# Kernel optimization log

Hardware: AMD Instinct MI355X
Metric: run time of the kernel (lower is better)

The kernel has to match this reference:

```python
import jax, jax.numpy as jnp
import numpy as np

L_SEQ = 4096   # sequence length L
E = 1024       # embedding_size
NL = 8         # num_layers
H = 4 * E      # channel-mix hidden
V = 4          # LocalHilDim
LOGP_FACTOR = 0.5


def setup_inputs() -> dict:
    key = jax.random.key(0)
    ks = jax.random.split(key, 20)
    n = lambda k, shp, s=0.02: jax.random.normal(k, shp, jnp.float32) * s
    u = lambda k, shp: jax.random.uniform(k, shp, dtype=jnp.float32)
    return {
        "s": jax.random.randint(ks[0], (L_SEQ,), 0, V),
        "embed": n(ks[1], (V, E), 1.0),
        # TimeMixing params, stacked over layers
        "tm_first": jnp.log(jnp.float32(0.3)) + n(ks[2], (NL, E), 0.5),
        "tm_decay": -5.0 + 8.0 * u(ks[3], (NL, E)),
        "tm_mk": u(ks[4], (NL, E)),
        "tm_mv": u(ks[5], (NL, E)),
        "tm_mr": u(ks[6], (NL, E)),
        "tm_Wk": n(ks[7], (NL, E, E)),
        "tm_Wv": n(ks[8], (NL, E, E)),
        "tm_Wr": n(ks[9], (NL, E, E)),
        "tm_Wo": n(ks[10], (NL, E, E)),
        # ChannelMixing params
        "cm_mk": u(ks[11], (NL, E)),
        "cm_mr": u(ks[12], (NL, E)),
        "cm_Wk": n(ks[13], (NL, E, H)),
        "cm_Wr": n(ks[14], (NL, E, E)),
        "cm_Wv": n(ks[15], (NL, H, E)),
        # Neck / Head
        "neck_W": n(ks[16], (E, E)),
        "neck_b": jnp.zeros((E,), jnp.float32),
        "head_W": n(ks[17], (E, V)),
    }


def _wkv(k, v, time_first, time_decay):
    """Max-stabilized RWKV WKV recurrence over time. k,v: [L,E]."""
    z = jnp.zeros_like(k[0])
    init = (z, z, jnp.full_like(k[0], -jnp.inf))  # aa, bb, pp

    def step(carry, kv):
        aa, bb, pp = carry
        kk, vv = kv
        ww = time_first + kk
        p = jnp.maximum(pp, ww)
        e1 = jnp.exp(pp - p)
        e2 = jnp.exp(ww - p)
        out = (e1 * aa + e2 * vv) / (e1 * bb + e2)
        ww = pp - jnp.exp(time_decay)
        p = jnp.maximum(ww, kk)
        e1 = jnp.exp(ww - p)
        e2 = jnp.exp(kk - p)
        return (e1 * aa + e2 * vv, e1 * bb + e2, p), out

    _, out = jax.lax.scan(step, init, (k, v))
    return out


def _shift(x):
    # prepend zero-state row, drop last (token-shift with zero initial state)
    return jnp.concatenate([jnp.zeros_like(x[:1]), x[:-1]], axis=0)


def _block(x, p):
    # --- TimeMixing ---
    sx = _shift(x)
    kx = x * p["tm_mk"] + sx * (1 - p["tm_mk"])
    vx = x * p["tm_mv"] + sx * (1 - p["tm_mv"])
    rx = x * p["tm_mr"] + sx * (1 - p["tm_mr"])
    r = jax.nn.sigmoid(rx @ p["tm_Wr"])
    k = kx @ p["tm_Wk"]
    v = vx @ p["tm_Wv"]
    wkv = _wkv(k, v, p["tm_first"], p["tm_decay"])
    x = x + (r * wkv) @ p["tm_Wo"]
    # --- ChannelMixing ---
    sx = _shift(x)
    xk = x * p["cm_mk"] + sx * (1 - p["cm_mk"])
    xr = x * p["cm_mr"] + sx * (1 - p["cm_mr"])
    r = jax.nn.sigmoid(xr @ p["cm_Wr"])
    kk = jnp.square(jax.nn.relu(xk @ p["cm_Wk"]))  # [L, 4E]
    x = x + r * (kk @ p["cm_Wv"])
    return x


def reference(s, embed, tm_first, tm_decay, tm_mk, tm_mv, tm_mr,
              tm_Wk, tm_Wv, tm_Wr, tm_Wo, cm_mk, cm_mr, cm_Wk, cm_Wr, cm_Wv,
              neck_W, neck_b, head_W):
    tok = jnp.pad(s[:-1], (1, 0))
    x = embed[tok]                          # [L, E]
    layer_params = {
        "tm_first": tm_first, "tm_decay": tm_decay,
        "tm_mk": tm_mk, "tm_mv": tm_mv, "tm_mr": tm_mr,
        "tm_Wk": tm_Wk, "tm_Wv": tm_Wv, "tm_Wr": tm_Wr, "tm_Wo": tm_Wo,
        "cm_mk": cm_mk, "cm_mr": cm_mr,
        "cm_Wk": cm_Wk, "cm_Wr": cm_Wr, "cm_Wv": cm_Wv,
    }

    def body(x, p):
        return _block(x, p), None

    x, _ = jax.lax.scan(body, x, layer_params)  # scan over NL layers
    x = jax.nn.gelu(x @ neck_W + neck_b)
    logits = x @ head_W                         # [L, V]
    logp = jax.nn.log_softmax(logits) * LOGP_FACTOR
    # log-amplitude of configuration s (Q is None -> no mask, no penalty)
    return jnp.take_along_axis(logp, s[:, None], axis=-1).sum(axis=-2).squeeze(-1)
```

## Files before the change

kernel.cpp:

```cpp
#include <hip/hip_runtime.h>
#include <stdint.h>

#define L_SEQ 4096
#define EDIM  1024
#define HDIM  4096
#define NLAY  8
#define WKV_C 128
#define WKV_T 32
#define SCAN_LANES 16
#define SCAN_CPT   (WKV_C / SCAN_LANES)

typedef unsigned short u16;
typedef __attribute__((ext_vector_type(8))) short short8;
typedef __attribute__((ext_vector_type(4))) float f32x4;
typedef __attribute__((ext_vector_type(4))) unsigned short us4;

static __device__ __forceinline__ u16 f2b(float f) {
  union { float f; uint32_t u; } a; a.f = f;
  uint32_t u = a.u;
  return (u16)((u + 0x7FFFu + ((u >> 16) & 1u)) >> 16);
}
static __device__ __forceinline__ float b2f(u16 b) {
  union { uint32_t u; float f; } a; a.u = ((uint32_t)b) << 16;
  return a.f;
}
static __device__ __forceinline__ float sigm(float v) {
  return 1.f / (1.f + __expf(-v));
}
static __device__ __forceinline__ float4 ld_bf4(const u16* __restrict__ p, size_t i) {
  us4 v = *reinterpret_cast<const us4*>(&p[i]);
  return make_float4(b2f(v.x), b2f(v.y), b2f(v.z), b2f(v.w));
}

static __device__ __forceinline__ void gld_lds16(const void* g, void* l) {
  __builtin_amdgcn_global_load_lds(
      (const __attribute__((address_space(1))) void*)g,
      (__attribute__((address_space(3))) void*)l, 16, 0, 0);
}


__global__ void k_f0(const int* __restrict__ s, const float* __restrict__ embed,
                     const float* __restrict__ mk, const float* __restrict__ mv,
                     const float* __restrict__ mr, float* __restrict__ xA,
                     u16* __restrict__ kx, u16* __restrict__ vx, u16* __restrict__ rx) {
  int i = (blockIdx.x * blockDim.x + threadIdx.x) * 4;
  int t = i >> 10, e = i & 1023;
  int tok = (t == 0) ? 0 : s[t - 1];
  float4 xc = *reinterpret_cast<const float4*>(&embed[tok * EDIM + e]);
  float4 xs = make_float4(0.f, 0.f, 0.f, 0.f);
  if (t > 0) {
    int tokp = (t == 1) ? 0 : s[t - 2];
    xs = *reinterpret_cast<const float4*>(&embed[tokp * EDIM + e]);
  }
  *reinterpret_cast<float4*>(&xA[i]) = xc;
  float4 m; us4 o;
  m = *reinterpret_cast<const float4*>(&mk[e]);
  o.x = f2b(xc.x * m.x + xs.x * (1.f - m.x)); o.y = f2b(xc.y * m.y + xs.y * (1.f - m.y));
  o.z = f2b(xc.z * m.z + xs.z * (1.f - m.z)); o.w = f2b(xc.w * m.w + xs.w * (1.f - m.w));
  *reinterpret_cast<us4*>(&kx[i]) = o;
  m = *reinterpret_cast<const float4*>(&mv[e]);
  o.x = f2b(xc.x * m.x + xs.x * (1.f - m.x)); o.y = f2b(xc.y * m.y + xs.y * (1.f - m.y));
  o.z = f2b(xc.z * m.z + xs.z * (1.f - m.z)); o.w = f2b(xc.w * m.w + xs.w * (1.f - m.w));
  *reinterpret_cast<us4*>(&vx[i]) = o;
  m = *reinterpret_cast<const float4*>(&mr[e]);
  o.x = f2b(xc.x * m.x + xs.x * (1.f - m.x)); o.y = f2b(xc.y * m.y + xs.y * (1.f - m.y));
  o.z = f2b(xc.z * m.z + xs.z * (1.f - m.z)); o.w = f2b(xc.w * m.w + xs.w * (1.f - m.w));
  *reinterpret_cast<us4*>(&rx[i]) = o;
}

static __device__ __forceinline__ float4 cm_finish(const float* __restrict__ xB,
                                                   const u16* __restrict__ PR,
                                                   const u16* __restrict__ PB, int i) {
  const size_t LE = (size_t)L_SEQ * EDIM;
  float4 xm = *reinterpret_cast<const float4*>(&xB[i]);
  float4 r0 = ld_bf4(PR, i), r1 = ld_bf4(PR, i + LE);
  float4 v0 = ld_bf4(PB, i), v1 = ld_bf4(PB, i + LE);
  float4 v2 = ld_bf4(PB, i + 2 * LE), v3 = ld_bf4(PB, i + 3 * LE);
  xm.x += sigm(r0.x + r1.x) * (v0.x + v1.x + v2.x + v3.x);
  xm.y += sigm(r0.y + r1.y) * (v0.y + v1.y + v2.y + v3.y);
  xm.z += sigm(r0.z + r1.z) * (v0.z + v1.z + v2.z + v3.z);
  xm.w += sigm(r0.w + r1.w) * (v0.w + v1.w + v2.w + v3.w);
  return xm;
}

__global__ void k_f1(const float* __restrict__ xB, const u16* __restrict__ PR,
                     const u16* __restrict__ PB,
                     const float* __restrict__ mk, const float* __restrict__ mv,
                     const float* __restrict__ mr, float* __restrict__ xA,
                     u16* __restrict__ kx, u16* __restrict__ vx, u16* __restrict__ rx) {
  int i = (blockIdx.x * blockDim.x + threadIdx.x) * 4;
  int e = i & 1023;
  float4 xc = cm_finish(xB, PR, PB, i);
  float4 xs = make_float4(0.f, 0.f, 0.f, 0.f);
  if (i >= EDIM) xs = cm_finish(xB, PR, PB, i - EDIM);
  *reinterpret_cast<float4*>(&xA[i]) = xc;
  float4 m; us4 o;
  m = *reinterpret_cast<const float4*>(&mk[e]);
  o.x = f2b(xc.x * m.x + xs.x * (1.f - m.x)); o.y = f2b(xc.y * m.y + xs.y * (1.f - m.y));
  o.z = f2b(xc.z * m.z + xs.z * (1.f - m.z)); o.w = f2b(xc.w * m.w + xs.w * (1.f - m.w));
  *reinterpret_cast<us4*>(&kx[i]) = o;
  m = *reinterpret_cast<const float4*>(&mv[e]);
  o.x = f2b(xc.x * m.x + xs.x * (1.f - m.x)); o.y = f2b(xc.y * m.y + xs.y * (1.f - m.y));
  o.z = f2b(xc.z * m.z + xs.z * (1.f - m.z)); o.w = f2b(xc.w * m.w + xs.w * (1.f - m.w));
  *reinterpret_cast<us4*>(&vx[i]) = o;
  m = *reinterpret_cast<const float4*>(&mr[e]);
  o.x = f2b(xc.x * m.x + xs.x * (1.f - m.x)); o.y = f2b(xc.y * m.y + xs.y * (1.f - m.y));
  o.z = f2b(xc.z * m.z + xs.z * (1.f - m.z)); o.w = f2b(xc.w * m.w + xs.w * (1.f - m.w));
  *reinterpret_cast<us4*>(&rx[i]) = o;
}

static __device__ __forceinline__ float4 tm_finish(const float* __restrict__ xA,
                                                   const u16* __restrict__ PA, int i) {
  const size_t LE = (size_t)L_SEQ * EDIM;
  float4 xm = *reinterpret_cast<const float4*>(&xA[i]);
  float4 a = ld_bf4(PA, i), b = ld_bf4(PA, i + LE);
  xm.x += a.x + b.x; xm.y += a.y + b.y; xm.z += a.z + b.z; xm.w += a.w + b.w;
  return xm;
}

__global__ void k_f2(const float* __restrict__ xA, const u16* __restrict__ PA,
                     const float* __restrict__ mk, const float* __restrict__ mr,
                     float* __restrict__ xB, u16* __restrict__ kx, u16* __restrict__ rx) {
  int i = (blockIdx.x * blockDim.x + threadIdx.x) * 4;
  int e = i & 1023;
  float4 xc = tm_finish(xA, PA, i);
  float4 xs = make_float4(0.f, 0.f, 0.f, 0.f);
  if (i >= EDIM) xs = tm_finish(xA, PA, i - EDIM);
  *reinterpret_cast<float4*>(&xB[i]) = xc;
  float4 m; us4 o;
  m = *reinterpret_cast<const float4*>(&mk[e]);
  o.x = f2b(xc.x * m.x + xs.x * (1.f - m.x)); o.y = f2b(xc.y * m.y + xs.y * (1.f - m.y));
  o.z = f2b(xc.z * m.z + xs.z * (1.f - m.z)); o.w = f2b(xc.w * m.w + xs.w * (1.f - m.w));
  *reinterpret_cast<us4*>(&kx[i]) = o;
  m = *reinterpret_cast<const float4*>(&mr[e]);
  o.x = f2b(xc.x * m.x + xs.x * (1.f - m.x)); o.y = f2b(xc.y * m.y + xs.y * (1.f - m.y));
  o.z = f2b(xc.z * m.z + xs.z * (1.f - m.z)); o.w = f2b(xc.w * m.w + xs.w * (1.f - m.w));
  *reinterpret_cast<us4*>(&rx[i]) = o;
}

__global__ void k_f3(const float* __restrict__ xB, const u16* __restrict__ PR,
                     const u16* __restrict__ PB, u16* __restrict__ hb) {
  int i = (blockIdx.x * blockDim.x + threadIdx.x) * 4;
  float4 xc = cm_finish(xB, PR, PB, i);
  us4 o;
  o.x = f2b(xc.x); o.y = f2b(xc.y); o.z = f2b(xc.z); o.w = f2b(xc.w);
  *reinterpret_cast<us4*>(&hb[i]) = o;
}

static __device__ __forceinline__ float gelu1(float v) {
  float c = 0.7978845608028654f * (v + 0.044715f * v * v * v);
  return 0.5f * v * (1.f + tanhf(c));
}

static __device__ __forceinline__
void tconv_body(const float* __restrict__ s, u16* __restrict__ d, int K, int N) {
  __shared__ float tile[64][65];
  int n0 = blockIdx.x * 64, k0 = blockIdx.y * 64;
  int tx = threadIdx.x & 15, ty = threadIdx.x >> 4;
#pragma unroll
  for (int i = 0; i < 4; ++i) {
    int kr = ty + i * 16;
    float4 v = *reinterpret_cast<const float4*>(&s[(size_t)(k0 + kr) * N + n0 + tx * 4]);
    tile[kr][tx * 4 + 0] = v.x; tile[kr][tx * 4 + 1] = v.y;
    tile[kr][tx * 4 + 2] = v.z; tile[kr][tx * 4 + 3] = v.w;
  }
  __syncthreads();
#pragma unroll
  for (int i = 0; i < 4; ++i) {
    int nr = ty + i * 16;
    us4 o;
    o.x = f2b(tile[tx * 4 + 0][nr]); o.y = f2b(tile[tx * 4 + 1][nr]);
    o.z = f2b(tile[tx * 4 + 2][nr]); o.w = f2b(tile[tx * 4 + 3][nr]);
    *reinterpret_cast<us4*>(&d[(size_t)(n0 + nr) * K + k0 + tx * 4]) = o;
  }
}

__global__ __launch_bounds__(256)
void k_tconv(const float* __restrict__ src, u16* __restrict__ dst, int K, int N) {
  tconv_body(src + (size_t)blockIdx.z * K * N, dst + (size_t)blockIdx.z * K * N, K, N);
}

__global__ __launch_bounds__(256)
void k_tconv_ee(const float* __restrict__ Wk, const float* __restrict__ Wv,
                const float* __restrict__ Wr, const float* __restrict__ Wo,
                const float* __restrict__ cWr, const float* __restrict__ nW,
                u16* __restrict__ oWk, u16* __restrict__ oWv, u16* __restrict__ oWr,
                u16* __restrict__ oWo, u16* __restrict__ ocWr, u16* __restrict__ onW) {
  const size_t EE = (size_t)EDIM * EDIM;
  int z = blockIdx.z;
  const float* src; u16* dst;
  if (z < 8)       { src = Wk  + (size_t)z * EE;        dst = oWk  + (size_t)z * EE; }
  else if (z < 16) { src = Wv  + (size_t)(z - 8) * EE;  dst = oWv  + (size_t)(z - 8) * EE; }
  else if (z < 24) { src = Wr  + (size_t)(z - 16) * EE; dst = oWr  + (size_t)(z - 16) * EE; }
  else if (z < 32) { src = Wo  + (size_t)(z - 24) * EE; dst = oWo  + (size_t)(z - 24) * EE; }
  else if (z < 40) { src = cWr + (size_t)(z - 32) * EE; dst = ocWr + (size_t)(z - 32) * EE; }
  else             { src = nW;                          dst = onW; }
  tconv_body(src, dst, EDIM, EDIM);
}

template <int EPI>
__device__ __forceinline__
void g256_body(const u16* __restrict__ A, const u16* __restrict__ Bt,
               void* __restrict__ Cv, int N, int ldk, int klen,
               int bm, int bn) {
  extern __shared__ __align__(16) u16 lds[];
  const int tid = threadIdx.x, lane = tid & 63, w = tid >> 6;
  const int wr = w >> 2, wc = w & 3;
  const int l16 = lane & 15, lhi = lane >> 4;
  const int NT = klen >> 5;

  f32x4 acc[8][4];
#pragma unroll
  for (int i = 0; i < 8; ++i)
#pragma unroll
    for (int j = 0; j < 4; ++j)
#pragma unroll
      for (int r = 0; r < 4; ++r) acc[i][j][r] = 0.f;

  const int sd = tid * 16;
  const int sr = sd >> 6;
  const int sc = ((sd >> 4) & 3) ^ ((sr >> 1) & 3);
  const int sdst = w * 512;

  const int spn = lhi ^ ((l16 >> 1) & 3);
  const int aBase = wr * 4096 + l16 * 32 + spn * 8;
  const int bBase = 8192 + (wc >> 1) * 4096 + ((wc & 1) * 64 + l16) * 32 + spn * 8;

  auto stage_ht = [&](int kt, int ht) {
    const u16* src = (ht < 2) ? A : Bt;
    int rowbase = ((ht < 2) ? bm : bn) + (ht & 1) * 128;
    gld_lds16(src + (size_t)(rowbase + sr) * ldk + kt * 32 + sc * 8,
              &lds[(kt & 3) * 16384 + ht * 4096 + sdst]);
  };

#pragma unroll
  for (int t = 0; t < 3; ++t)
#pragma unroll
    for (int h = 0; h < 4; ++h) stage_ht(t, h);
  asm volatile("s_waitcnt vmcnt(8)" ::: "memory");
  __builtin_amdgcn_s_barrier();

  short8 a[4], b[4];
  for (int kt = 0; kt < NT; ++kt) {
    const int pb = (kt & 3) * 16384;
    __builtin_amdgcn_sched_barrier(0);
#pragma unroll
    for (int mi = 0; mi < 4; ++mi)
      a[mi] = *reinterpret_cast<const short8*>(&lds[pb + aBase + mi * 512]);
#pragma unroll
    for (int ni = 0; ni < 4; ++ni)
      b[ni] = *reinterpret_cast<const short8*>(&lds[pb + bBase + ni * 512]);
    if (kt + 3 < NT) { stage_ht(kt + 3, 0); stage_ht(kt + 3, 1); }
    __builtin_amdgcn_s_barrier();
    asm volatile("s_waitcnt lgkmcnt(0)" ::: "memory");
    __builtin_amdgcn_sched_barrier(0);
    __builtin_amdgcn_s_setprio(1);
#pragma unroll
    for (int mi = 0; mi < 4; ++mi)
#pragma unroll
      for (int ni = 0; ni < 4; ++ni)
        acc[mi][ni] = __builtin_amdgcn_mfma_f32_16x16x32_bf16(a[mi], b[ni], acc[mi][ni], 0, 0, 0);
    __builtin_amdgcn_s_setprio(0);
    __builtin_amdgcn_s_barrier();
    __builtin_amdgcn_sched_barrier(0);
#pragma unroll
    for (int mi = 0; mi < 4; ++mi)
      a[mi] = *reinterpret_cast<const short8*>(&lds[pb + aBase + 2048 + mi * 512]);
    if (kt + 3 < NT) { stage_ht(kt + 3, 2); stage_ht(kt + 3, 3); }
    __builtin_amdgcn_s_barrier();
    asm volatile("s_waitcnt lgkmcnt(0)" ::: "memory");
    __builtin_amdgcn_sched_barrier(0);
    __builtin_amdgcn_s_setprio(1);
#pragma unroll
    for (int mi = 0; mi < 4; ++mi)
#pragma unroll
      for (int ni = 0; ni < 4; ++ni)
        acc[4 + mi][ni] = __builtin_amdgcn_mfma_f32_16x16x32_bf16(a[mi], b[ni], acc[4 + mi][ni], 0, 0, 0);
    __builtin_amdgcn_s_setprio(0);
    if (kt + 4 <= NT)      asm volatile("s_waitcnt vmcnt(8)" ::: "memory");
    else if (kt + 3 == NT) asm volatile("s_waitcnt vmcnt(4)" ::: "memory");
    else if (kt + 2 == NT) asm volatile("s_waitcnt vmcnt(0)" ::: "memory");
    __builtin_amdgcn_s_barrier();
  }

#pragma unroll
  for (int q = 0; q < 8; ++q)
#pragma unroll
    for (int ni = 0; ni < 4; ++ni)
#pragma unroll
      for (int r = 0; r < 4; ++r) {
        int row = bm + wr * 128 + (q >> 2) * 64 + (q & 3) * 16 + lhi * 4 + r;
        int col = bn + wc * 64 + ni * 16 + l16;
        size_t o = (size_t)row * N + col;
        float v = acc[q][ni][r];
        if constexpr (EPI == 0) ((float*)Cv)[o] = v;
        else if constexpr (EPI == 1) ((u16*)Cv)[o] = f2b(v);
        else { v = fmaxf(v, 0.f); ((u16*)Cv)[o] = f2b(v * v); }
      }
}

__global__ __launch_bounds__(512)
void k_g256_cmk(const u16* __restrict__ A, const u16* __restrict__ Bt,
                u16* __restrict__ C) {
  int bid = blockIdx.x;
  int wg = (bid & 7) * 32 + (bid >> 3);
  int lb = wg & 3, sv = wg >> 2;
  int by = (sv >> 3) * 2 + (lb & 1);
  int bx = (sv & 7) * 2 + (lb >> 1);
  g256_body<2>(A, Bt, C, HDIM, EDIM, EDIM, by * 256, bx * 256);
}

__global__ __launch_bounds__(512)
void k_g256_wv(const u16* __restrict__ A, const u16* __restrict__ Bt,
               u16* __restrict__ P) {
  int bid = blockIdx.x;
  int wg = (bid & 7) * 32 + (bid >> 3);
  int z = wg >> 6, rem = wg & 63;
  int lb = rem & 3, sv = rem >> 2;
  int by = (sv >> 1) * 2 + (lb & 1);
  int bx = (sv & 1) * 2 + (lb >> 1);
  g256_body<1>(A + z * 1024, Bt + z * 1024, P + (size_t)z * L_SEQ * EDIM,
               EDIM, HDIM, 1024, by * 256, bx * 256);
}

__global__ __launch_bounds__(512)
void k_g256_3(const u16* __restrict__ A0, const u16* __restrict__ A1, const u16* __restrict__ A2,
              const u16* __restrict__ B0, const u16* __restrict__ B1, const u16* __restrict__ B2,
              u16* __restrict__ C0, u16* __restrict__ C1, u16* __restrict__ C2) {
  int bid = blockIdx.x;
  int wg = (bid & 7) * 24 + (bid >> 3);
  int z = wg >> 6, rem = wg & 63;
  int lb = rem & 3, sv = rem >> 2;
  int by = (sv >> 1) * 2 + (lb & 1);
  int bx = (sv & 1) * 2 + (lb >> 1);
  const u16* A = (z == 0) ? A0 : (z == 1) ? A1 : A2;
  const u16* B = (z == 0) ? B0 : (z == 1) ? B1 : B2;
  u16*       C = (z == 0) ? C0 : (z == 1) ? C1 : C2;
  g256_body<1>(A, B, C, EDIM, EDIM, EDIM, by * 256, bx * 256);
}

__device__ __forceinline__
void gemm_body(const u16* __restrict__ A, const u16* __restrict__ Bt,
               u16* __restrict__ Cv, int N, int ldk, int klen, int bm, int bn) {
  __shared__ __align__(16) u16 As[4][128 * 32];
  __shared__ __align__(16) u16 Bs[4][128 * 32];
  const int tid = threadIdx.x, lane = tid & 63, w = tid >> 6;
  const int wr = w >> 1, wc = w & 1;
  const int l16 = lane & 15, lhi = lane >> 4;

  f32x4 acc[4][4];
#pragma unroll
  for (int a = 0; a < 4; ++a)
#pragma unroll
    for (int b = 0; b < 4; ++b)
#pragma unroll
      for (int r = 0; r < 4; ++r) acc[a][b][r] = 0.f;

  const size_t rowBytes = (size_t)ldk * 2;
  const int NT = klen >> 5;

  int srow[2], scb[2], ldso[2];
#pragma unroll
  for (int i = 0; i < 2; ++i) {
    int off = w * 2048 + i * 1024 + lane * 16;
    int r = off >> 6, sl = (off >> 4) & 3;
    srow[i] = r;
    scb[i] = ((sl - (r >> 1)) & 3) << 4;
    ldso[i] = (w * 2048 + i * 1024) >> 1;
  }

  auto stage = [&](int t, int buf) {
    int kb = t * 64;
#pragma unroll
    for (int i = 0; i < 2; ++i) {
      gld_lds16((const char*)A + (size_t)(bm + srow[i]) * rowBytes + kb + scb[i],
                &As[buf][ldso[i]]);
      gld_lds16((const char*)Bt + (size_t)(bn + srow[i]) * rowBytes + kb + scb[i],
                &Bs[buf][ldso[i]]);
    }
  };

  int aoff[4], boff[4];
#pragma unroll
  for (int mi = 0; mi < 4; ++mi) {
    int r = wr * 64 + mi * 16 + l16;
    aoff[mi] = r * 32 + (((lhi + (r >> 1)) & 3) << 3);
    r = wc * 64 + mi * 16 + l16;
    boff[mi] = r * 32 + (((lhi + (r >> 1)) & 3) << 3);
  }

  stage(0, 0); stage(1, 1); stage(2, 2);
  for (int t = 0; t < NT; ++t) {
    const int cur = t & 3;
    if (t + 2 < NT)      asm volatile("s_waitcnt vmcnt(8)" ::: "memory");
    else if (t + 1 < NT) asm volatile("s_waitcnt vmcnt(4)" ::: "memory");
    else                 asm volatile("s_waitcnt vmcnt(0)" ::: "memory");
    __builtin_amdgcn_s_barrier();
    __builtin_amdgcn_sched_barrier(0);
    short8 af[4], bfr[4];
#pragma unroll
    for (int mi = 0; mi < 4; ++mi)
      af[mi] = *reinterpret_cast<const short8*>(&As[cur][aoff[mi]]);
#pragma unroll
    for (int ni = 0; ni < 4; ++ni)
      bfr[ni] = *reinterpret_cast<const short8*>(&Bs[cur][boff[ni]]);
    if (t + 3 < NT) stage(t + 3, (t + 3) & 3);
    asm volatile("s_waitcnt lgkmcnt(0)" ::: "memory");
    __builtin_amdgcn_sched_barrier(0);
#pragma unroll
    for (int mi = 0; mi < 4; ++mi)
#pragma unroll
      for (int ni = 0; ni < 4; ++ni)
        acc[mi][ni] = __builtin_amdgcn_mfma_f32_16x16x32_bf16(af[mi], bfr[ni], acc[mi][ni], 0, 0, 0);
  }
#pragma unroll
  for (int mi = 0; mi < 4; ++mi)
#pragma unroll
    for (int ni = 0; ni < 4; ++ni)
#pragma unroll
      for (int r = 0; r < 4; ++r) {
        int row = bm + wr * 64 + mi * 16 + lhi * 4 + r;
        int col = bn + wc * 64 + ni * 16 + l16;
        Cv[(size_t)row * N + col] = f2b(acc[mi][ni][r]);
      }
}

__global__ __launch_bounds__(256)
void k_gemm_sk2(const u16* __restrict__ A, const u16* __restrict__ Bt,
                u16* __restrict__ P, int K) {
  const int z = blockIdx.z, klen = K >> 1;
  gemm_body(A + z * klen, Bt + z * klen, P + (size_t)z * L_SEQ * EDIM,
            EDIM, K, klen, blockIdx.y * 128, blockIdx.x * 128);
}


__global__ void k_wkv_pass1(const u16* __restrict__ k, const u16* __restrict__ v,
                            const float* __restrict__ w_,
                            float* __restrict__ sa, float* __restrict__ sb,
                            float* __restrict__ sp) {
  int id = blockIdx.x * blockDim.x + threadIdx.x;
  int e = id & 1023, c = id >> 10;
  float D = __expf(w_[e]);
  float aa = 0.f, bb = 0.f, pp = -__builtin_inff();
  const u16* kp = k + (size_t)c * WKV_T * EDIM + e;
  const u16* vp = v + (size_t)c * WKV_T * EDIM + e;
#pragma unroll 4
  for (int i = 0; i < WKV_T; ++i) {
    float kk = b2f(kp[i * EDIM]), vv = b2f(vp[i * EDIM]);
    float ww = pp - D;
    float p2 = fmaxf(ww, kk);
    float e1 = __expf(ww - p2), e2 = __expf(kk - p2);
    aa = e1 * aa + e2 * vv;
    bb = e1 * bb + e2;
    pp = p2;
  }
  sa[id] = aa; sb[id] = bb; sp[id] = pp;
}

__global__ __launch_bounds__(256)
void k_wkv_scan16(const float* __restrict__ w_,
                  const float* __restrict__ sa, const float* __restrict__ sb,
                  const float* __restrict__ sp,
                  float* __restrict__ oa, float* __restrict__ ob,
                  float* __restrict__ op) {
  int t = blockIdx.x * blockDim.x + threadIdx.x;
  int e = t >> 4, j = t & (SCAN_LANES - 1);
  const float NEG = -1e30f;
  float DT = __expf(w_[e]) * (float)WKV_T;
  float Ea[SCAN_CPT], Eb[SCAN_CPT], Ep[SCAN_CPT];
  float A = 0.f, B = 0.f, P = NEG;
  int base = j * SCAN_CPT;
#pragma unroll
  for (int i = 0; i < SCAN_CPT; ++i) {
    int idx = (base + i) * EDIM + e;
    Ea[i] = A; Eb[i] = B; Ep[i] = P;
    float a = sa[idx], b = sb[idx], q = sp[idx];
    float shift = P - DT;
    float pn = fmaxf(shift, q);
    float w1 = __expf(shift - pn), w2 = __expf(q - pn);
    A = w1 * A + w2 * a; B = w1 * B + w2 * b; P = pn;
  }
  float tA = A, tB = B, tP = P; int tn = SCAN_CPT;
#pragma unroll
  for (int d = 1; d < SCAN_LANES; d <<= 1) {
    float fA = __shfl_up(tA, d, SCAN_LANES);
    float fB = __shfl_up(tB, d, SCAN_LANES);
    float fP = __shfl_up(tP, d, SCAN_LANES);
    int   fn = __shfl_up(tn, d, SCAN_LANES);
    if (j >= d) {
      float shift = fP - DT * (float)tn;
      float pn = fmaxf(shift, tP);
      float w1 = __expf(shift - pn), w2 = __expf(tP - pn);
      tA = w1 * fA + w2 * tA; tB = w1 * fB + w2 * tB; tP = pn; tn += fn;
    }
  }
  float pA = __shfl_up(tA, 1, SCAN_LANES);
  float pB = __shfl_up(tB, 1, SCAN_LANES);
  float pP = __shfl_up(tP, 1, SCAN_LANES);
  if (j == 0) { pA = 0.f; pB = 0.f; pP = NEG; }
#pragma unroll
  for (int i = 0; i < SCAN_CPT; ++i) {
    float shift = pP - DT * (float)i;
    float pn = fmaxf(shift, Ep[i]);
    float w1 = __expf(shift - pn), w2 = __expf(Ep[i] - pn);
    int idx = (base + i) * EDIM + e;
    oa[idx] = w1 * pA + w2 * Ea[i];
    ob[idx] = w1 * pB + w2 * Eb[i];
    op[idx] = pn;
  }
}

__global__ void k_wkv_pass2(const u16* __restrict__ k, const u16* __restrict__ v,
                            const float* __restrict__ u_, const float* __restrict__ w_,
                            const float* __restrict__ sa, const float* __restrict__ sb,
                            const float* __restrict__ sp,
                            const u16* __restrict__ rpre, u16* __restrict__ rwb) {
  int id = blockIdx.x * blockDim.x + threadIdx.x;
  int e = id & 1023, c = id >> 10;
  float u = u_[e];
  float D = __expf(w_[e]);
  float aa = sa[id], bb = sb[id], pp = sp[id];
  const size_t base = (size_t)c * WKV_T * EDIM + e;
  const u16* kp = k + base;
  const u16* vp = v + base;
  const u16* rp = rpre + base;
  u16* op = rwb + base;
#pragma unroll 4
  for (int i = 0; i < WKV_T; ++i) {
    float kk = b2f(kp[i * EDIM]), vv = b2f(vp[i * EDIM]);
    float ww = u + kk;
    float p = fmaxf(pp, ww);
    float e1 = __expf(pp - p), e2 = __expf(ww - p);
    float out = (e1 * aa + e2 * vv) / (e1 * bb + e2);
    op[i * EDIM] = f2b(out * sigm(b2f(rp[i * EDIM])));
    float w2s = pp - D;
    float p2 = fmaxf(w2s, kk);
    float e1b = __expf(w2s - p2), e2b = __expf(kk - p2);
    aa = e1b * aa + e2b * vv;
    bb = e1b * bb + e2b;
    pp = p2;
  }
}

__global__ __launch_bounds__(256)
void k_head(const u16* __restrict__ P, const float* __restrict__ nb,
            const float* __restrict__ W,
            const int* __restrict__ s, float* __restrict__ partial) {
  const size_t LE = (size_t)L_SEQ * EDIM;
  int t = blockIdx.x, tid = threadIdx.x;
  float a0 = 0.f, a1 = 0.f, a2 = 0.f, a3 = 0.f;
  for (int e = tid; e < EDIM; e += 256) {
    size_t i = (size_t)t * EDIM + e;
    float hv = gelu1(b2f(P[i]) + b2f(P[i + LE]) + nb[e]);
    const float4 wv = *reinterpret_cast<const float4*>(W + e * 4);
    a0 += hv * wv.x; a1 += hv * wv.y; a2 += hv * wv.z; a3 += hv * wv.w;
  }
#pragma unroll
  for (int off = 32; off > 0; off >>= 1) {
    a0 += __shfl_down(a0, off, 64);
    a1 += __shfl_down(a1, off, 64);
    a2 += __shfl_down(a2, off, 64);
    a3 += __shfl_down(a3, off, 64);
  }
  __shared__ float sm[4][4];
  int w = tid >> 6, lane = tid & 63;
  if (lane == 0) { sm[w][0] = a0; sm[w][1] = a1; sm[w][2] = a2; sm[w][3] = a3; }
  __syncthreads();
  if (tid == 0) {
    float lg[4];
#pragma unroll
    for (int j = 0; j < 4; ++j) lg[j] = sm[0][j] + sm[1][j] + sm[2][j] + sm[3][j];
    float m = fmaxf(fmaxf(lg[0], lg[1]), fmaxf(lg[2], lg[3]));
    float sum = expf(lg[0] - m) + expf(lg[1] - m) + expf(lg[2] - m) + expf(lg[3] - m);
    partial[t] = 0.5f * (lg[s[t]] - m - logf(sum));
  }
}

__global__ __launch_bounds__(256)
void k_reduce(const float* __restrict__ partial, float* __restrict__ out) {
  int tid = threadIdx.x;
  float a = 0.f;
  for (int j = tid; j < L_SEQ; j += 256) a += partial[j];
#pragma unroll
  for (int off = 32; off > 0; off >>= 1) a += __shfl_down(a, off, 64);
  __shared__ float sm[4];
  if ((tid & 63) == 0) sm[tid >> 6] = a;
  __syncthreads();
  if (tid == 0) out[0] = sm[0] + sm[1] + sm[2] + sm[3];
}


extern "C" void kernel_launch(void* const* d_in, const int* in_sizes, int n_in,
                              void* d_out, int out_size, void* d_ws, size_t ws_size,
                              hipStream_t stream) {
  const int*   s        = (const int*)d_in[0];
  const float* embed    = (const float*)d_in[1];
  const float* tm_first = (const float*)d_in[2];
  const float* tm_decay = (const float*)d_in[3];
  const float* tm_mk    = (const float*)d_in[4];
  const float* tm_mv    = (const float*)d_in[5];
  const float* tm_mr    = (const float*)d_in[6];
  const float* tm_Wk    = (const float*)d_in[7];
  const float* tm_Wv    = (const float*)d_in[8];
  const float* tm_Wr    = (const float*)d_in[9];
  const float* tm_Wo    = (const float*)d_in[10];
  const float* cm_mk    = (const float*)d_in[11];
  const float* cm_mr    = (const float*)d_in[12];
  const float* cm_Wk    = (const float*)d_in[13];
  const float* cm_Wr    = (const float*)d_in[14];
  const float* cm_Wv    = (const float*)d_in[15];
  const float* neck_W   = (const float*)d_in[16];
  const float* neck_b   = (const float*)d_in[17];
  const float* head_W   = (const float*)d_in[18];

  char* ws = (char*)d_ws;
  size_t off = 0;
  auto alloc = [&](size_t bytes) { char* p = ws + off; off += (bytes + 255) & ~(size_t)255; return p; };
  const size_t LE4 = (size_t)L_SEQ * EDIM * 4, LE2 = (size_t)L_SEQ * EDIM * 2;
  const size_t EE  = (size_t)EDIM * EDIM, EH = (size_t)EDIM * HDIM;

  float* xA    = (float*)alloc(LE4);
  float* xB    = (float*)alloc(LE4);
  u16*   kxb   = (u16*)alloc(LE2);
  u16*   vxb   = (u16*)alloc(LE2);
  u16*   rxb   = (u16*)alloc(LE2);
  u16*   kf    = (u16*)alloc(LE2);
  u16*   vf    = (u16*)alloc(LE2);
  u16*   rpre  = (u16*)alloc(LE2);
  u16*   kkb   = (u16*)alloc((size_t)L_SEQ * HDIM * 2);
  u16*   PA    = (u16*)alloc(2 * LE2);
  u16*   PR    = (u16*)alloc(2 * LE2);
  u16*   PB    = (u16*)alloc(4 * LE2);
  float* partial = (float*)alloc((size_t)L_SEQ * 4);
  float* sa  = (float*)alloc((size_t)WKV_C * EDIM * 4);
  float* sb  = (float*)alloc((size_t)WKV_C * EDIM * 4);
  float* sp  = (float*)alloc((size_t)WKV_C * EDIM * 4);
  float* sa2 = (float*)alloc((size_t)WKV_C * EDIM * 4);
  float* sb2 = (float*)alloc((size_t)WKV_C * EDIM * 4);
  float* sp2 = (float*)alloc((size_t)WKV_C * EDIM * 4);

  size_t remain = (ws_size > off) ? ws_size - off : 0;
  const size_t bigNeed = (5 * EE * NLAY + 2 * EH * NLAY + EE) * 2 + 16 * 256;
  const bool big = remain >= bigNeed;
  const int NB = big ? NLAY : 1;
  u16* wWk   = (u16*)alloc(EE * NB * 2);
  u16* wWv   = (u16*)alloc(EE * NB * 2);
  u16* wWr   = (u16*)alloc(EE * NB * 2);
  u16* wWo   = (u16*)alloc(EE * NB * 2);
  u16* wcmWr = (u16*)alloc(EE * NB * 2);
  u16* wcmWk = (u16*)alloc(EH * NB * 2);
  u16* wcmWv = (u16*)alloc(EH * NB * 2);
  u16* wneck = big ? (u16*)alloc(EE * 2) : wWk;

  const dim3 blk(256);
  const dim3 blk512(512);
  const dim3 gE4((L_SEQ * EDIM) / 1024);
  const dim3 gemmSK(EDIM / 128, L_SEQ / 128, 2);
  const dim3 gWkv((WKV_C * EDIM) / 256);
  const dim3 gScan((EDIM * SCAN_LANES) / 256);
  const size_t DLDS = 131072;

  if (big) {
    k_tconv_ee<<<dim3(EDIM / 64, EDIM / 64, 41), blk, 0, stream>>>(
        tm_Wk, tm_Wv, tm_Wr, tm_Wo, cm_Wr, neck_W,
        wWk, wWv, wWr, wWo, wcmWr, wneck);
    k_tconv<<<dim3(HDIM / 64, EDIM / 64, NLAY), blk, 0, stream>>>(cm_Wk, wcmWk, EDIM, HDIM);
    k_tconv<<<dim3(EDIM / 64, HDIM / 64, NLAY), blk, 0, stream>>>(cm_Wv, wcmWv, HDIM, EDIM);
  }

  for (int l = 0; l < NLAY; ++l) {
    size_t oE  = (size_t)l * EDIM;
    size_t oEE = (size_t)l * EE;
    size_t oEH = (size_t)l * EH;
    size_t wE  = big ? oEE : 0;
    size_t wH  = big ? oEH : 0;
    if (!big) {
      k_tconv<<<dim3(EDIM / 64, EDIM / 64, 1), blk, 0, stream>>>(tm_Wk + oEE, wWk, EDIM, EDIM);
      k_tconv<<<dim3(EDIM / 64, EDIM / 64, 1), blk, 0, stream>>>(tm_Wv + oEE, wWv, EDIM, EDIM);
      k_tconv<<<dim3(EDIM / 64, EDIM / 64, 1), blk, 0, stream>>>(tm_Wr + oEE, wWr, EDIM, EDIM);
      k_tconv<<<dim3(EDIM / 64, EDIM / 64, 1), blk, 0, stream>>>(tm_Wo + oEE, wWo, EDIM, EDIM);
      k_tconv<<<dim3(EDIM / 64, EDIM / 64, 1), blk, 0, stream>>>(cm_Wr + oEE, wcmWr, EDIM, EDIM);
      k_tconv<<<dim3(HDIM / 64, EDIM / 64, 1), blk, 0, stream>>>(cm_Wk + oEH, wcmWk, EDIM, HDIM);
      k_tconv<<<dim3(EDIM / 64, HDIM / 64, 1), blk, 0, stream>>>(cm_Wv + oEH, wcmWv, HDIM, EDIM);
    }
    if (l == 0)
      k_f0<<<gE4, blk, 0, stream>>>(s, embed, tm_mk + oE, tm_mv + oE, tm_mr + oE,
                                    xA, kxb, vxb, rxb);
    else
      k_f1<<<gE4, blk, 0, stream>>>(xB, PR, PB, tm_mk + oE, tm_mv + oE, tm_mr + oE,
                                    xA, kxb, vxb, rxb);
    k_g256_3<<<dim3(192), blk512, DLDS, stream>>>(kxb, vxb, rxb,
                                                  wWk + wE, wWv + wE, wWr + wE,
                                                  kf, vf, rpre);
    k_wkv_pass1<<<gWkv, blk, 0, stream>>>(kf, vf, tm_decay + oE, sa, sb, sp);
    k_wkv_scan16<<<gScan, blk, 0, stream>>>(tm_decay + oE, sa, sb, sp, sa2, sb2, sp2);
    k_wkv_pass2<<<gWkv, blk, 0, stream>>>(kf, vf, tm_first + oE, tm_decay + oE,
                                          sa2, sb2, sp2, rpre, vxb);
    k_gemm_sk2<<<gemmSK, blk, 0, stream>>>(vxb, wWo + wE, PA, EDIM);
    k_f2<<<gE4, blk, 0, stream>>>(xA, PA, cm_mk + oE, cm_mr + oE, xB, kxb, rxb);
    k_gemm_sk2<<<gemmSK, blk, 0, stream>>>(rxb, wcmWr + wE, PR, EDIM);
    k_g256_cmk<<<dim3(256), blk512, DLDS, stream>>>(kxb, wcmWk + wH, kkb);
    k_g256_wv<<<dim3(256), blk512, DLDS, stream>>>(kkb, wcmWv + wH, PB);
  }
  if (!big) k_tconv<<<dim3(EDIM / 64, EDIM / 64, 1), blk, 0, stream>>>(neck_W, wneck, EDIM, EDIM);
  k_f3<<<gE4, blk, 0, stream>>>(xB, PR, PB, kxb);
  k_gemm_sk2<<<gemmSK, blk, 0, stream>>>(kxb, wneck, PA, EDIM);
  k_head<<<dim3(L_SEQ), blk, 0, stream>>>(PA, neck_b, head_W, s, partial);
  k_reduce<<<dim3(1), blk, 0, stream>>>(partial, (float*)d_out);

  (void)in_sizes; (void)n_in; (void)out_size;
}
```

Measured before the change: 1.888 ms.

## Store residual stream in bf16 and merge weight transpose-convert launches

The fp32 residual buffers xA/xB become bf16, which halves their global traffic in the elementwise finish kernels. The three weight transpose/convert launches are merged into one flat-grid kernel, and its store path now writes 8-wide bf16 vectors instead of 4-wide. In exchange, the residual stream is rounded to bf16 after every sublayer across all 8 layers, which adds accumulated rounding error and may threaten the accuracy tolerance.

```diff
diff --git a/kernel.cpp b/kernel.cpp
--- a/kernel.cpp
+++ b/kernel.cpp
@@ -14,6 +14,7 @@
 typedef __attribute__((ext_vector_type(8))) short short8;
 typedef __attribute__((ext_vector_type(4))) float f32x4;
 typedef __attribute__((ext_vector_type(4))) unsigned short us4;
+typedef __attribute__((ext_vector_type(8))) unsigned short us8;
 
 static __device__ __forceinline__ u16 f2b(float f) {
   union { float f; uint32_t u; } a; a.f = f;
@@ -41,7 +42,7 @@
 
 __global__ void k_f0(const int* __restrict__ s, const float* __restrict__ embed,
                      const float* __restrict__ mk, const float* __restrict__ mv,
-                     const float* __restrict__ mr, float* __restrict__ xA,
+                     const float* __restrict__ mr, u16* __restrict__ xA,
                      u16* __restrict__ kx, u16* __restrict__ vx, u16* __restrict__ rx) {
   int i = (blockIdx.x * blockDim.x + threadIdx.x) * 4;
   int t = i >> 10, e = i & 1023;
@@ -52,7 +53,8 @@
     int tokp = (t == 1) ? 0 : s[t - 2];
     xs = *reinterpret_cast<const float4*>(&embed[tokp * EDIM + e]);
   }
-  *reinterpret_cast<float4*>(&xA[i]) = xc;
+  us4 ox; ox.x = f2b(xc.x); ox.y = f2b(xc.y); ox.z = f2b(xc.z); ox.w = f2b(xc.w);
+  *reinterpret_cast<us4*>(&xA[i]) = ox;
   float4 m; us4 o;
   m = *reinterpret_cast<const float4*>(&mk[e]);
   o.x = f2b(xc.x * m.x + xs.x * (1.f - m.x)); o.y = f2b(xc.y * m.y + xs.y * (1.f - m.y));
@@ -68,11 +70,11 @@
   *reinterpret_cast<us4*>(&rx[i]) = o;
 }
 
-static __device__ __forceinline__ float4 cm_finish(const float* __restrict__ xB,
+static __device__ __forceinline__ float4 cm_finish(const u16* __restrict__ xB,
                                                    const u16* __restrict__ PR,
                                                    const u16* __restrict__ PB, int i) {
   const size_t LE = (size_t)L_SEQ * EDIM;
-  float4 xm = *reinterpret_cast<const float4*>(&xB[i]);
+  float4 xm = ld_bf4(xB, i);
   float4 r0 = ld_bf4(PR, i), r1 = ld_bf4(PR, i + LE);
   float4 v0 = ld_bf4(PB, i), v1 = ld_bf4(PB, i + LE);
   float4 v2 = ld_bf4(PB, i + 2 * LE), v3 = ld_bf4(PB, i + 3 * LE);
@@ -83,17 +85,18 @@
   return xm;
 }
 
-__global__ void k_f1(const float* __restrict__ xB, const u16* __restrict__ PR,
+__global__ void k_f1(const u16* __restrict__ xB, const u16* __restrict__ PR,
                      const u16* __restrict__ PB,
                      const float* __restrict__ mk, const float* __restrict__ mv,
-                     const float* __restrict__ mr, float* __restrict__ xA,
+                     const float* __restrict__ mr, u16* __restrict__ xA,
                      u16* __restrict__ kx, u16* __restrict__ vx, u16* __restrict__ rx) {
   int i = (blockIdx.x * blockDim.x + threadIdx.x) * 4;
   int e = i & 1023;
   float4 xc = cm_finish(xB, PR, PB, i);
   float4 xs = make_float4(0.f, 0.f, 0.f, 0.f);
   if (i >= EDIM) xs = cm_finish(xB, PR, PB, i - EDIM);
-  *reinterpret_cast<float4*>(&xA[i]) = xc;
+  us4 ox; ox.x = f2b(xc.x); ox.y = f2b(xc.y); ox.z = f2b(xc.z); ox.w = f2b(xc.w);
+  *reinterpret_cast<us4*>(&xA[i]) = ox;
   float4 m; us4 o;
   m = *reinterpret_cast<const float4*>(&mk[e]);
   o.x = f2b(xc.x * m.x + xs.x * (1.f - m.x)); o.y = f2b(xc.y * m.y + xs.y * (1.f - m.y));
@@ -109,24 +112,25 @@
   *reinterpret_cast<us4*>(&rx[i]) = o;
 }
 
-static __device__ __forceinline__ float4 tm_finish(const float* __restrict__ xA,
+static __device__ __forceinline__ float4 tm_finish(const u16* __restrict__ xA,
                                                    const u16* __restrict__ PA, int i) {
   const size_t LE = (size_t)L_SEQ * EDIM;
-  float4 xm = *reinterpret_cast<const float4*>(&xA[i]);
+  float4 xm = ld_bf4(xA, i);
   float4 a = ld_bf4(PA, i), b = ld_bf4(PA, i + LE);
   xm.x += a.x + b.x; xm.y += a.y + b.y; xm.z += a.z + b.z; xm.w += a.w + b.w;
   return xm;
 }
 
-__global__ void k_f2(const float* __restrict__ xA, const u16* __restrict__ PA,
+__global__ void k_f2(const u16* __restrict__ xA, const u16* __restrict__ PA,
                      const float* __restrict__ mk, const float* __restrict__ mr,
-                     float* __restrict__ xB, u16* __restrict__ kx, u16* __restrict__ rx) {
+                     u16* __restrict__ xB, u16* __restrict__ kx, u16* __restrict__ rx) {
   int i = (blockIdx.x * blockDim.x + threadIdx.x) * 4;
   int e = i & 1023;
   float4 xc = tm_finish(xA, PA, i);
   float4 xs = make_float4(0.f, 0.f, 0.f, 0.f);
   if (i >= EDIM) xs = tm_finish(xA, PA, i - EDIM);
-  *reinterpret_cast<float4*>(&xB[i]) = xc;
+  us4 ox; ox.x = f2b(xc.x); ox.y = f2b(xc.y); ox.z = f2b(xc.z); ox.w = f2b(xc.w);
+  *reinterpret_cast<us4*>(&xB[i]) = ox;
   float4 m; us4 o;
   m = *reinterpret_cast<const float4*>(&mk[e]);
   o.x = f2b(xc.x * m.x + xs.x * (1.f - m.x)); o.y = f2b(xc.y * m.y + xs.y * (1.f - m.y));
@@ -138,7 +142,7 @@
   *reinterpret_cast<us4*>(&rx[i]) = o;
 }
 
-__global__ void k_f3(const float* __restrict__ xB, const u16* __restrict__ PR,
+__global__ void k_f3(const u16* __restrict__ xB, const u16* __restrict__ PR,
                      const u16* __restrict__ PB, u16* __restrict__ hb) {
   int i = (blockIdx.x * blockDim.x + threadIdx.x) * 4;
   float4 xc = cm_finish(xB, PR, PB, i);
@@ -153,10 +157,11 @@
 }
 
 static __device__ __forceinline__
-void tconv_body(const float* __restrict__ s, u16* __restrict__ d, int K, int N) {
+void tconv2(const float* __restrict__ s, u16* __restrict__ d, int K, int N,
+            int n0, int k0) {
   __shared__ float tile[64][65];
-  int n0 = blockIdx.x * 64, k0 = blockIdx.y * 64;
-  int tx = threadIdx.x & 15, ty = threadIdx.x >> 4;
+  int tid = threadIdx.x;
+  int tx = tid & 15, ty = tid >> 4;
 #pragma unroll
   for (int i = 0; i < 4; ++i) {
     int kr = ty + i * 16;
@@ -165,37 +170,56 @@
     tile[kr][tx * 4 + 2] = v.z; tile[kr][tx * 4 + 3] = v.w;
   }
   __syncthreads();
-#pragma unroll
-  for (int i = 0; i < 4; ++i) {
-    int nr = ty + i * 16;
-    us4 o;
-    o.x = f2b(tile[tx * 4 + 0][nr]); o.y = f2b(tile[tx * 4 + 1][nr]);
-    o.z = f2b(tile[tx * 4 + 2][nr]); o.w = f2b(tile[tx * 4 + 3][nr]);
-    *reinterpret_cast<us4*>(&d[(size_t)(n0 + nr) * K + k0 + tx * 4]) = o;
+  int tx8 = tid & 7, ny = tid >> 3;
+#pragma unroll
+  for (int h = 0; h < 2; ++h) {
+    int n = ny + h * 32;
+    us8 o;
+#pragma unroll
+    for (int c = 0; c < 8; ++c) o[c] = f2b(tile[tx8 * 8 + c][n]);
+    *reinterpret_cast<us8*>(&d[(size_t)(n0 + n) * K + k0 + tx8 * 8]) = o;
   }
 }
 
 __global__ __launch_bounds__(256)
 void k_tconv(const float* __restrict__ src, u16* __restrict__ dst, int K, int N) {
-  tconv_body(src + (size_t)blockIdx.z * K * N, dst + (size_t)blockIdx.z * K * N, K, N);
-}
-
+  tconv2(src + (size_t)blockIdx.z * K * N, dst + (size_t)blockIdx.z * K * N,
+         K, N, blockIdx.x * 64, blockIdx.y * 64);
+}
+
+#define TC_EE  (41 * 256)
+#define TC_EH  8192
 __global__ __launch_bounds__(256)
-void k_tconv_ee(const float* __restrict__ Wk, const float* __restrict__ Wv,
-                const float* __restrict__ Wr, const float* __restrict__ Wo,
-                const float* __restrict__ cWr, const float* __restrict__ nW,
-                u16* __restrict__ oWk, u16* __restrict__ oWv, u16* __restrict__ oWr,
-                u16* __restrict__ oWo, u16* __restrict__ ocWr, u16* __restrict__ onW) {
-  const size_t EE = (size_t)EDIM * EDIM;
-  int z = blockIdx.z;
-  const float* src; u16* dst;
-  if (z < 8)       { src = Wk  + (size_t)z * EE;        dst = oWk  + (size_t)z * EE; }
-  else if (z < 16) { src = Wv  + (size_t)(z - 8) * EE;  dst = oWv  + (size_t)(z - 8) * EE; }
-  else if (z < 24) { src = Wr  + (size_t)(z - 16) * EE; dst = oWr  + (size_t)(z - 16) * EE; }
-  else if (z < 32) { src = Wo  + (size_t)(z - 24) * EE; dst = oWo  + (size_t)(z - 24) * EE; }
-  else if (z < 40) { src = cWr + (size_t)(z - 32) * EE; dst = ocWr + (size_t)(z - 32) * EE; }
-  else             { src = nW;                          dst = onW; }
-  tconv_body(src, dst, EDIM, EDIM);
+void k_tconv_all(const float* __restrict__ Wk, const float* __restrict__ Wv,
+                 const float* __restrict__ Wr, const float* __restrict__ Wo,
+                 const float* __restrict__ cWr, const float* __restrict__ nW,
+                 const float* __restrict__ cWk, const float* __restrict__ cWv,
+                 u16* __restrict__ oWk, u16* __restrict__ oWv, u16* __restrict__ oWr,
+                 u16* __restrict__ oWo, u16* __restrict__ ocWr, u16* __restrict__ onW,
+                 u16* __restrict__ ocWk, u16* __restrict__ ocWv) {
+  const size_t EE = (size_t)EDIM * EDIM, EH = (size_t)EDIM * HDIM;
+  int bid = blockIdx.x;
+  if (bid < TC_EE) {
+    int z = bid >> 8, rem = bid & 255;
+    const float* src; u16* dst;
+    if (z < 8)       { src = Wk  + (size_t)z * EE;        dst = oWk  + (size_t)z * EE; }
+    else if (z < 16) { src = Wv  + (size_t)(z - 8) * EE;  dst = oWv  + (size_t)(z - 8) * EE; }
+    else if (z < 24) { src = Wr  + (size_t)(z - 16) * EE; dst = oWr  + (size_t)(z - 16) * EE; }
+    else if (z < 32) { src = Wo  + (size_t)(z - 24) * EE; dst = oWo  + (size_t)(z - 24) * EE; }
+    else if (z < 40) { src = cWr + (size_t)(z - 32) * EE; dst = ocWr + (size_t)(z - 32) * EE; }
+    else             { src = nW;                          dst = onW; }
+    tconv2(src, dst, EDIM, EDIM, (rem & 15) * 64, (rem >> 4) * 64);
+  } else if (bid < TC_EE + TC_EH) {
+    int b = bid - TC_EE;
+    int z = b >> 10, rem = b & 1023;
+    tconv2(cWk + (size_t)z * EH, ocWk + (size_t)z * EH, EDIM, HDIM,
+           (rem & 63) * 64, (rem >> 6) * 64);
+  } else {
+    int b = bid - TC_EE - TC_EH;
+    int z = b >> 10, rem = b & 1023;
+    tconv2(cWv + (size_t)z * EH, ocWv + (size_t)z * EH, HDIM, EDIM,
+           (rem & 15) * 64, (rem >> 4) * 64);
+  }
 }
 
 template <int EPI>
@@ -616,11 +640,11 @@
   char* ws = (char*)d_ws;
   size_t off = 0;
   auto alloc = [&](size_t bytes) { char* p = ws + off; off += (bytes + 255) & ~(size_t)255; return p; };
-  const size_t LE4 = (size_t)L_SEQ * EDIM * 4, LE2 = (size_t)L_SEQ * EDIM * 2;
+  const size_t LE2 = (size_t)L_SEQ * EDIM * 2;
   const size_t EE  = (size_t)EDIM * EDIM, EH = (size_t)EDIM * HDIM;
 
-  float* xA    = (float*)alloc(LE4);
-  float* xB    = (float*)alloc(LE4);
+  u16*   xA    = (u16*)alloc(LE2);
+  u16*   xB    = (u16*)alloc(LE2);
   u16*   kxb   = (u16*)alloc(LE2);
   u16*   vxb   = (u16*)alloc(LE2);
   u16*   rxb   = (u16*)alloc(LE2);
@@ -661,11 +685,9 @@
   const size_t DLDS = 131072;
 
   if (big) {
-    k_tconv_ee<<<dim3(EDIM / 64, EDIM / 64, 41), blk, 0, stream>>>(
-        tm_Wk, tm_Wv, tm_Wr, tm_Wo, cm_Wr, neck_W,
-        wWk, wWv, wWr, wWo, wcmWr, wneck);
-    k_tconv<<<dim3(HDIM / 64, EDIM / 64, NLAY), blk, 0, stream>>>(cm_Wk, wcmWk, EDIM, HDIM);
-    k_tconv<<<dim3(EDIM / 64, HDIM / 64, NLAY), blk, 0, stream>>>(cm_Wv, wcmWv, HDIM, EDIM);
+    k_tconv_all<<<dim3(TC_EE + 2 * TC_EH), blk, 0, stream>>>(
+        tm_Wk, tm_Wv, tm_Wr, tm_Wo, cm_Wr, neck_W, cm_Wk, cm_Wv,
+        wWk, wWv, wWr, wWo, wcmWr, wneck, wcmWk, wcmWv);
   }
 
   for (int l = 0; l < NLAY; ++l) {
```

Result: faster. 1.849 ms (-2.1%).
